# Kernel tuning notes

Measured on AMD Instinct MI355X. Metric: run time of the kernel, lower is better.

The kernel has to match this reference:

```python
import jax, jax.numpy as jnp
import numpy as np

TAU = 1.0
K_TAU = 1.0
MAX_K = 64


def setup_inputs() -> dict:
    key = jax.random.key(0)
    ks = jax.random.split(key, 6)
    B, S, D, H = 8, 4096, 1024, 2048
    token_embeddings = jax.random.normal(ks[0], (B, S, D), dtype=jnp.float32)
    W1 = jax.random.normal(ks[1], (D, H), dtype=jnp.float32) * (1.0 / np.sqrt(D))
    b1 = jnp.zeros((H,), dtype=jnp.float32)
    W2 = jax.random.normal(ks[2], (H, 1), dtype=jnp.float32) * (1.0 / np.sqrt(H))
    b2 = jnp.zeros((1,), dtype=jnp.float32)
    k_logits = jax.random.normal(ks[3], (MAX_K,), dtype=jnp.float32) * 0.02
    return {"token_embeddings": token_embeddings, "W1": W1, "b1": b1,
            "W2": W2, "b2": b2, "k_logits": k_logits}


def _gumbel(rng, shape):
    u = jax.random.uniform(rng, shape, minval=1e-08, maxval=1.0 - 1e-08)
    return -jnp.log(-jnp.log(u))


def reference(token_embeddings, W1, b1, W2, b2, k_logits):
    B, S, D = token_embeddings.shape
    # scorer: Dense -> relu -> Dense(1), squeeze -> [B, S]
    h = jax.nn.relu(jnp.einsum('bsd,dh->bsh', token_embeddings, W1) + b1)
    importance_logits = (jnp.einsum('bsh,ho->bso', h, W2) + b2)[..., 0]

    rng = jax.random.key(42)  # training rng
    rng1, rng2 = jax.random.split(rng)

    # learnable-k selection (training branch)
    k_gumbel = _gumbel(rng1, k_logits.shape)
    k_soft = jax.nn.softmax((k_logits + k_gumbel) / K_TAU)
    expected_k = jnp.sum(k_soft * jnp.arange(1, MAX_K + 1, dtype=k_soft.dtype))
    k_selected = jnp.argmax(k_soft) + 1  # traced int scalar

    # gumbel-softmax hard top-k over tokens
    perturbed = importance_logits + _gumbel(rng2, importance_logits.shape)
    soft_mask = jax.nn.softmax(perturbed / TAU, axis=-1)  # [B, S]
    # rank of each token (0 = smallest); top-k == rank >= S - k
    rank = jnp.argsort(jnp.argsort(soft_mask, axis=-1), axis=-1)
    hard_mask = (rank >= S - k_selected).astype(soft_mask.dtype)
    selection_mask = jax.lax.stop_gradient(hard_mask - soft_mask) + soft_mask

    filtered_embeddings = token_embeddings * selection_mask[..., None]
    return filtered_embeddings, selection_mask, expected_k
```

## Files before the change

kernel.cpp:

```cpp
#include <hip/hip_runtime.h>
#include <stdint.h>

#define B_BATCH 8
#define S_SEQ   4096
#define D_DIM   1024
#define H_DIM   2048
#define M_TOK   (B_BATCH * S_SEQ)
#define MAXK    64
#define NSPLIT  2

typedef unsigned int u32;
typedef unsigned short u16;
typedef unsigned long long u64;
typedef __attribute__((ext_vector_type(8))) short short8;
typedef __attribute__((ext_vector_type(4))) float f32x4;

#define GLOBAL_AS __attribute__((address_space(1)))
#define LDS_AS    __attribute__((address_space(3)))


#define TF_ROUND(x0, x1, r) { x0 += x1; x1 = ((x1 << r) | (x1 >> (32 - r))); x1 ^= x0; }

__device__ __forceinline__ void tf2x32(u32 k0, u32 k1, u32 x0, u32 x1, u32& o0, u32& o1) {
  u32 k2 = k0 ^ k1 ^ 0x1BD11BDAu;
  x0 += k0; x1 += k1;
  TF_ROUND(x0, x1, 13) TF_ROUND(x0, x1, 15) TF_ROUND(x0, x1, 26) TF_ROUND(x0, x1, 6)
  x0 += k1; x1 += k2 + 1u;
  TF_ROUND(x0, x1, 17) TF_ROUND(x0, x1, 29) TF_ROUND(x0, x1, 16) TF_ROUND(x0, x1, 24)
  x0 += k2; x1 += k0 + 2u;
  TF_ROUND(x0, x1, 13) TF_ROUND(x0, x1, 15) TF_ROUND(x0, x1, 26) TF_ROUND(x0, x1, 6)
  x0 += k0; x1 += k1 + 3u;
  TF_ROUND(x0, x1, 17) TF_ROUND(x0, x1, 29) TF_ROUND(x0, x1, 16) TF_ROUND(x0, x1, 24)
  x0 += k1; x1 += k2 + 4u;
  TF_ROUND(x0, x1, 13) TF_ROUND(x0, x1, 15) TF_ROUND(x0, x1, 26) TF_ROUND(x0, x1, 6)
  x0 += k2; x1 += k0 + 5u;
  o0 = x0; o1 = x1;
}

__device__ __forceinline__ void jax_subkeys(u32& r1a, u32& r1b, u32& r2a, u32& r2b) {
  tf2x32(0u, 42u, 0u, 0u, r1a, r1b);
  tf2x32(0u, 42u, 0u, 1u, r2a, r2b);
}

__device__ __forceinline__ u32 jax_bits32(u32 ka, u32 kb, u32 i) {
  u32 o0, o1;
  tf2x32(ka, kb, 0u, i, o0, o1);
  return o0 ^ o1;
}

__device__ __forceinline__ float jax_uniform_from_bits(u32 bits) {
  float f = __uint_as_float((bits >> 9) | 0x3f800000u) - 1.0f;
  float r = f + 1e-8f;
  return fmaxf(1e-8f, r);
}

__device__ __forceinline__ float gumbel_from_bits(u32 bits) {
  float u = jax_uniform_from_bits(bits);
  return -logf(-logf(u));
}

__device__ __forceinline__ u32 ordf(float v) {
  u32 b = __float_as_uint(v);
  return (b & 0x80000000u) ? ~b : (b | 0x80000000u);
}

__device__ __forceinline__ u64 shflx64(u64 v, int m) {
  unsigned lo = (unsigned)v, hi = (unsigned)(v >> 32);
  lo = (unsigned)__shfl_xor((int)lo, m);
  hi = (unsigned)__shfl_xor((int)hi, m);
  return ((u64)hi << 32) | lo;
}


__device__ __forceinline__ u16 f2bf_rn(float x) {
  u32 u = __float_as_uint(x);
  u32 r = u + 0x7fffu + ((u >> 16) & 1u);
  return (u16)(r >> 16);
}

__device__ __forceinline__ void split1(float x, u16& h, u16& lo) {
  h = f2bf_rn(x);
  float hf = __uint_as_float(((u32)h) << 16);
  lo = f2bf_rn(x - hf);
}


__global__ __launch_bounds__(256) void split_a_kernel(const float* __restrict__ x,
                                                      u16* __restrict__ hi,
                                                      u16* __restrict__ lo) {
  const size_t i = ((size_t)blockIdx.x * 256 + threadIdx.x) * 4;
  float4 v = *(const float4*)(x + i);
  u16 h0, h1, h2, h3, l0, l1, l2, l3;
  split1(v.x, h0, l0); split1(v.y, h1, l1); split1(v.z, h2, l2); split1(v.w, h3, l3);
  u64 hv = (u64)h0 | ((u64)h1 << 16) | ((u64)h2 << 32) | ((u64)h3 << 48);
  u64 lv = (u64)l0 | ((u64)l1 << 16) | ((u64)l2 << 32) | ((u64)l3 << 48);
  *(u64*)(hi + i) = hv;
  *(u64*)(lo + i) = lv;
}

__global__ __launch_bounds__(256) void split_w1t_kernel(const float* __restrict__ W1,
                                                        u16* __restrict__ bhi,
                                                        u16* __restrict__ blo) {
  __shared__ float tile[32][33];
  const int tx = threadIdx.x & 31, ty = threadIdx.x >> 5;
  const int n0 = blockIdx.x * 32, k0 = blockIdx.y * 32;
  #pragma unroll
  for (int r = 0; r < 4; ++r)
    tile[ty + r * 8][tx] = W1[(size_t)(k0 + ty + r * 8) * H_DIM + n0 + tx];
  __syncthreads();
  #pragma unroll
  for (int r = 0; r < 4; ++r) {
    const int n = n0 + ty + r * 8, k = k0 + tx;
    u16 h, l;
    split1(tile[tx][ty + r * 8], h, l);
    bhi[(size_t)n * D_DIM + k] = h;
    blo[(size_t)n * D_DIM + k] = l;
  }
}


__device__ __forceinline__ void stage16(const u16* g, u16* l) {
  __builtin_amdgcn_global_load_lds((const GLOBAL_AS u32*)g, (LDS_AS u32*)l, 16, 0, 0);
}

#define WAITV(N) asm volatile("s_waitcnt vmcnt(" #N ")" ::: "memory")
#define FENCE()  asm volatile("" ::: "memory")

__global__ __launch_bounds__(512, 2) void scorer_mfma256(
    const u16* __restrict__ Ahi, const u16* __restrict__ Alo,
    const u16* __restrict__ Bhi, const u16* __restrict__ Blo,
    const float* __restrict__ b1, const float* __restrict__ W2,
    float* __restrict__ pl) {
  extern __shared__ u16 smem[];
  float* red = (float*)(smem + 65536);

  const int tid = threadIdx.x;
  const int w = tid >> 6, l = tid & 63;
  const int wm = w >> 2, wn = w & 3;

  const int b = blockIdx.x;
  const int xcd = b & 7;
  const int nyb = xcd & 1;
  const int m0 = ((b >> 3) * 4 + (xcd >> 1)) * 256;

  const int sig = w * 16 + (l >> 2);
  const int swz = ((l & 3) ^ ((sig >> 1) & 3)) << 3;
  const size_t aoffE = (size_t)(m0 + sig + (sig & 64)) * D_DIM + swz;
  const size_t aoffL = aoffE + (size_t)64 * D_DIM;
  const size_t boff0 = (size_t)(nyb * 1024 + sig) * D_DIM + swz;
  const size_t boff1 = boff0 + (size_t)128 * D_DIM;
  u16* const ldsw = smem + w * 512;

#define ST_AhiE(T) stage16(Ahi + aoffE + (size_t)((((T) & 31) << 5)), ldsw + (((T) & 1) << 15) + 0)
#define ST_AhiL(T) stage16(Ahi + aoffL + (size_t)((((T) & 31) << 5)), ldsw + (((T) & 1) << 15) + 4096)
#define ST_AloE(T) stage16(Alo + aoffE + (size_t)((((T) & 31) << 5)), ldsw + (((T) & 1) << 15) + 8192)
#define ST_AloL(T) stage16(Alo + aoffL + (size_t)((((T) & 31) << 5)), ldsw + (((T) & 1) << 15) + 12288)
#define ST_BhiH0(T) stage16(Bhi + boff0 + ((size_t)((T) >> 5) << 18) + (size_t)((((T) & 31) << 5)), ldsw + (((T) & 1) << 15) + 16384)
#define ST_BhiH1(T) stage16(Bhi + boff1 + ((size_t)((T) >> 5) << 18) + (size_t)((((T) & 31) << 5)), ldsw + (((T) & 1) << 15) + 20480)
#define ST_BloH0(T) stage16(Blo + boff0 + ((size_t)((T) >> 5) << 18) + (size_t)((((T) & 31) << 5)), ldsw + (((T) & 1) << 15) + 24576)
#define ST_BloH1(T) stage16(Blo + boff1 + ((size_t)((T) >> 5) << 18) + (size_t)((((T) & 31) << 5)), ldsw + (((T) & 1) << 15) + 28672)

  int a_off[8], b_off[4];
  #pragma unroll
  for (int mf = 0; mf < 8; ++mf) {
    int slot = wm * 64 + (mf & 3) * 16 + (l & 15);
    a_off[mf] = ((mf >> 2) * 4096) + slot * 32 + (((l >> 4) ^ ((slot >> 1) & 3)) << 3);
  }
  #pragma unroll
  for (int nf = 0; nf < 4; ++nf) {
    int r = wn * 64 + nf * 16 + (l & 15);
    b_off[nf] = r * 32 + (((l >> 4) ^ ((r >> 1) & 3)) << 3);
  }

  f32x4 acc[8][4];
  #pragma unroll
  for (int mf = 0; mf < 8; ++mf)
    #pragma unroll
    for (int nf = 0; nf < 4; ++nf) acc[mf][nf] = (f32x4){0.f, 0.f, 0.f, 0.f};

  const u16* const B0 = smem;
  const u16* const B1 = smem + 32768;
  short8 ah0, ah1, al0, al1, bh[4], bl[4];

#define LDA(BASE, MF) \
  ah0 = *(const short8*)((BASE) + a_off[MF]); \
  ah1 = *(const short8*)((BASE) + a_off[(MF) + 1]); \
  al0 = *(const short8*)((BASE) + 8192 + a_off[MF]); \
  al1 = *(const short8*)((BASE) + 8192 + a_off[(MF) + 1])

#define LDB(BASE) \
  { _Pragma("unroll") \
    for (int nf = 0; nf < 4; ++nf) { \
      bh[nf] = *(const short8*)((BASE) + 16384 + b_off[nf]); \
      bl[nf] = *(const short8*)((BASE) + 24576 + b_off[nf]); \
    } }

#define MMA2(MF) \
  __builtin_amdgcn_s_setprio(1); \
  { _Pragma("unroll") \
    for (int nf = 0; nf < 4; ++nf) { \
      acc[MF][nf] = __builtin_amdgcn_mfma_f32_16x16x32_bf16(ah0, bh[nf], acc[MF][nf], 0, 0, 0); \
      acc[MF][nf] = __builtin_amdgcn_mfma_f32_16x16x32_bf16(ah0, bl[nf], acc[MF][nf], 0, 0, 0); \
      acc[MF][nf] = __builtin_amdgcn_mfma_f32_16x16x32_bf16(al0, bh[nf], acc[MF][nf], 0, 0, 0); \
      acc[(MF) + 1][nf] = __builtin_amdgcn_mfma_f32_16x16x32_bf16(ah1, bh[nf], acc[(MF) + 1][nf], 0, 0, 0); \
      acc[(MF) + 1][nf] = __builtin_amdgcn_mfma_f32_16x16x32_bf16(ah1, bl[nf], acc[(MF) + 1][nf], 0, 0, 0); \
      acc[(MF) + 1][nf] = __builtin_amdgcn_mfma_f32_16x16x32_bf16(al1, bh[nf], acc[(MF) + 1][nf], 0, 0, 0); \
    } } \
  __builtin_amdgcn_s_setprio(0)

  ST_BhiH0(0); ST_BhiH1(0); ST_BloH0(0); ST_BloH1(0);
  ST_AhiE(0);  ST_AloE(0);  ST_AhiL(0);  ST_AloL(0);
  ST_BhiH0(1); ST_BhiH1(1); ST_BloH0(1); ST_BloH1(1);
  ST_AhiE(1);  ST_AloE(1);
  WAITV(8);
  __builtin_amdgcn_s_barrier();
  FENCE();

  for (int it = 0; it < 64; ++it) {
    const bool last = (it == 63);
    const int T1 = 2 * it + 1, T2 = 2 * it + 2, T3 = 2 * it + 3;

    LDB(B0); LDA(B0, 0);
    ST_AhiL(T1); ST_AloL(T1);
    MMA2(0);
    __builtin_amdgcn_s_barrier(); FENCE();
    LDA(B0, 2);
    if (!last) { ST_BhiH0(T2); ST_BhiH1(T2); }
    MMA2(2);
    if (last) { WAITV(8); } else { WAITV(10); }
    __builtin_amdgcn_s_barrier(); FENCE();
    LDA(B0, 4);
    if (!last) { ST_BloH0(T2); ST_BloH1(T2); }
    MMA2(4);
    __builtin_amdgcn_s_barrier(); FENCE();
    LDA(B0, 6);
    if (!last) { ST_AhiE(T2); ST_AloE(T2); }
    MMA2(6);
    if (last) { WAITV(2); } else { WAITV(8); }
    __builtin_amdgcn_s_barrier(); FENCE();
    LDB(B1); LDA(B1, 0);
    if (!last) { ST_AhiL(T2); ST_AloL(T2); }
    MMA2(0);
    __builtin_amdgcn_s_barrier(); FENCE();
    LDA(B1, 2);
    if (!last) { ST_BhiH0(T3); ST_BhiH1(T3); }
    MMA2(2);
    if (last) { WAITV(0); } else { WAITV(10); }
    __builtin_amdgcn_s_barrier(); FENCE();
    LDA(B1, 4);
    if (!last) { ST_BloH0(T3); ST_BloH1(T3); }
    MMA2(4);
    __builtin_amdgcn_s_barrier(); FENCE();
    LDA(B1, 6);
    if (!last) { ST_AhiE(T3); ST_AloE(T3); }
    MMA2(6);

    if ((it & 15) == 15) {
      const int t8 = it >> 4;
      const int nb = nyb * 1024 + t8 * 256 + wn * 64 + (l & 15);
      float b1v[4], w2v[4];
      #pragma unroll
      for (int nf = 0; nf < 4; ++nf) { b1v[nf] = b1[nb + nf * 16]; w2v[nf] = W2[nb + nf * 16]; }
      #pragma unroll
      for (int mf = 0; mf < 8; ++mf)
        #pragma unroll
        for (int r = 0; r < 4; ++r) {
          float p = 0.f;
          #pragma unroll
          for (int nf = 0; nf < 4; ++nf)
            p += fmaxf(acc[mf][nf][r] + b1v[nf], 0.f) * w2v[nf];
          p += __shfl_xor(p, 1); p += __shfl_xor(p, 2);
          p += __shfl_xor(p, 4); p += __shfl_xor(p, 8);
          if ((l & 15) == 0) {
            float* rp = red + ((wm * 128 + mf * 16 + (l >> 4) * 4 + r) << 2) + wn;
            if (t8 == 0) *rp = p; else *rp += p;
          }
        }
      #pragma unroll
      for (int mf = 0; mf < 8; ++mf)
        #pragma unroll
        for (int nf = 0; nf < 4; ++nf) acc[mf][nf] = (f32x4){0.f, 0.f, 0.f, 0.f};
    }

    WAITV(8);
    __builtin_amdgcn_s_barrier(); FENCE();
  }

  __syncthreads();
  if (tid < 256) {
    const float* rp = red + (tid << 2);
    pl[(size_t)nyb * M_TOK + m0 + tid] = rp[0] + rp[1] + rp[2] + rp[3];
  }
}


__global__ __launch_bounds__(256) void scorer_kernel(
    const float* __restrict__ emb, const float* __restrict__ W1,
    const float* __restrict__ b1, const float* __restrict__ W2,
    const float* __restrict__ b2, float* __restrict__ pert) {
  __shared__ float As[16][68];
  __shared__ float Bs[16][132];
  __shared__ float red[64][17];

  const int tid = threadIdx.x;
  const int tx = tid & 15;
  const int ty = tid >> 4;
  const int m0 = blockIdx.x * 64;
  const int at = tid >> 2;
  const int ac = (tid & 3) << 2;
  const int br = tid >> 4;
  const int bc = (tid & 15) << 3;

  float logit[4] = {0.f, 0.f, 0.f, 0.f};

  for (int n0 = 0; n0 < H_DIM; n0 += 128) {
    float acc[4][8];
    #pragma unroll
    for (int i = 0; i < 4; i++)
      #pragma unroll
      for (int j = 0; j < 8; j++) acc[i][j] = 0.f;

    for (int k0 = 0; k0 < D_DIM; k0 += 16) {
      float4 av  = *(const float4*)(emb + (size_t)(m0 + at) * D_DIM + (k0 + ac));
      float4 bv0 = *(const float4*)(W1 + (size_t)(k0 + br) * H_DIM + (n0 + bc));
      float4 bv1 = *(const float4*)(W1 + (size_t)(k0 + br) * H_DIM + (n0 + bc) + 4);
      __syncthreads();
      As[ac + 0][at] = av.x; As[ac + 1][at] = av.y;
      As[ac + 2][at] = av.z; As[ac + 3][at] = av.w;
      *(float4*)&Bs[br][bc]     = bv0;
      *(float4*)&Bs[br][bc + 4] = bv1;
      __syncthreads();
      #pragma unroll
      for (int k = 0; k < 16; k++) {
        float4 a   = *(const float4*)&As[k][ty << 2];
        float4 b0  = *(const float4*)&Bs[k][tx << 3];
        float4 b1v = *(const float4*)&Bs[k][(tx << 3) + 4];
        float aa[4] = {a.x, a.y, a.z, a.w};
        float bb[8] = {b0.x, b0.y, b0.z, b0.w, b1v.x, b1v.y, b1v.z, b1v.w};
        #pragma unroll
        for (int i = 0; i < 4; i++)
          #pragma unroll
          for (int j = 0; j < 8; j++)
            acc[i][j] = fmaf(aa[i], bb[j], acc[i][j]);
      }
    }
    float4 c0 = *(const float4*)(b1 + n0 + (tx << 3));
    float4 c1 = *(const float4*)(b1 + n0 + (tx << 3) + 4);
    float4 w0 = *(const float4*)(W2 + n0 + (tx << 3));
    float4 w1 = *(const float4*)(W2 + n0 + (tx << 3) + 4);
    float cb[8] = {c0.x, c0.y, c0.z, c0.w, c1.x, c1.y, c1.z, c1.w};
    float wb[8] = {w0.x, w0.y, w0.z, w0.w, w1.x, w1.y, w1.z, w1.w};
    #pragma unroll
    for (int i = 0; i < 4; i++)
      #pragma unroll
      for (int j = 0; j < 8; j++) {
        float h = fmaxf(acc[i][j] + cb[j], 0.f);
        logit[i] = fmaf(h, wb[j], logit[i]);
      }
  }

  __syncthreads();
  #pragma unroll
  for (int i = 0; i < 4; i++) red[(ty << 2) + i][tx] = logit[i];
  __syncthreads();

  if (tid < 64) {
    float s = 0.f;
    #pragma unroll
    for (int x = 0; x < 16; x++) s += red[tid][x];
    s += b2[0];
    int t = m0 + tid;
    u32 r1a, r1b, r2a, r2b;
    jax_subkeys(r1a, r1b, r2a, r2b);
    pert[t] = s + gumbel_from_bits(jax_bits32(r2a, r2b, (u32)t));
  }
}


template <bool FROM_PL>
__device__ __forceinline__ void topk_body(const float* kl, const float* pl,
                                          const float* b2, float* mask,
                                          float* expk) {
  const int r = blockIdx.x;
  const int tid = threadIdx.x;
  const int w = tid >> 6, l = tid & 63;
  __shared__ int ksel_sh;
  __shared__ int cnt[2][4];

  u32 r1a, r1b, r2a, r2b;
  jax_subkeys(r1a, r1b, r2a, r2b);

  if (tid < 64) {
    float p = kl[l] + gumbel_from_bits(jax_bits32(r1a, r1b, (u32)l));
    u64 kkey = ((u64)ordf(p) << 32) | (unsigned)(63 - l);
    #pragma unroll
    for (int off = 32; off >= 1; off >>= 1) {
      u64 o = shflx64(kkey, off);
      if (o > kkey) kkey = o;
    }
    if (l == 0) ksel_sh = 64 - (int)(kkey & 0xffffffffu);
    if (r == 0) {
      float m = p;
      #pragma unroll
      for (int off = 32; off >= 1; off >>= 1) m = fmaxf(m, __shfl_xor(m, off));
      float e = expf(p - m);
      float s = e;
      #pragma unroll
      for (int off = 32; off >= 1; off >>= 1) s += __shfl_xor(s, off);
      float v = (e / s) * (float)(l + 1);
      #pragma unroll
      for (int off = 32; off >= 1; off >>= 1) v += __shfl_xor(v, off);
      if (l == 0) expk[0] = v;
    }
  }
  __syncthreads();
  const int k = ksel_sh;
  const float b2v = FROM_PL ? b2[0] : 0.f;

  u64 keys[16];
  #pragma unroll
  for (int j = 0; j < 16; j++) {
    int s = tid + (j << 8);
    int t = (r << 12) + s;
    float v;
    if (FROM_PL) {
      float acc = pl[t];
      #pragma unroll
      for (int q = 1; q < NSPLIT; ++q) acc += pl[(size_t)q * M_TOK + t];
      v = acc + b2v + gumbel_from_bits(jax_bits32(r2a, r2b, (u32)t));
    } else {
      v = mask[t];
    }
    keys[j] = ((u64)ordf(v) << 12) | (unsigned)s;
  }

  u64 lo = 0ull, hi = (1ull << 44) - 1ull;
  int it = 0;
  while (lo < hi) {
    const u64 mid = (lo + hi + 1ull) >> 1;
    int c = 0;
    #pragma unroll
    for (int j = 0; j < 16; j++) c += (keys[j] >= mid) ? 1 : 0;
    #pragma unroll
    for (int off = 32; off >= 1; off >>= 1) c += __shfl_xor(c, off);
    const int buf = it & 1;
    if (l == 0) cnt[buf][w] = c;
    __syncthreads();
    const int tot = cnt[buf][0] + cnt[buf][1] + cnt[buf][2] + cnt[buf][3];
    if (tot >= k) lo = mid; else hi = mid - 1ull;
    ++it;
  }
  const u64 thresh = lo;

  #pragma unroll
  for (int j = 0; j < 16; j++) {
    int s = tid + (j << 8);
    mask[(r << 12) + s] = (keys[j] >= thresh) ? 1.0f : 0.0f;
  }
}

__global__ __launch_bounds__(256) void topk_pl_kernel(const float* __restrict__ kl,
                                                      const float* __restrict__ pl,
                                                      const float* __restrict__ b2,
                                                      float* __restrict__ mask,
                                                      float* __restrict__ expk) {
  topk_body<true>(kl, pl, b2, mask, expk);
}

__global__ __launch_bounds__(256) void topk_kernel(const float* __restrict__ kl,
                                                   float* __restrict__ mask,
                                                   float* __restrict__ expk) {
  topk_body<false>(kl, nullptr, nullptr, mask, expk);
}


__global__ __launch_bounds__(256) void filter_kernel(const float* __restrict__ emb,
                                                     const float* __restrict__ mask,
                                                     float* __restrict__ out) {
  const int t = blockIdx.x;
  const float mk = mask[t];
  const size_t base = (size_t)t * D_DIM + ((size_t)threadIdx.x << 2);
  float4 v = *(const float4*)(emb + base);
  *(float4*)(out + base) = make_float4(v.x * mk, v.y * mk, v.z * mk, v.w * mk);
}


extern "C" void kernel_launch(void* const* d_in, const int* in_sizes, int n_in,
                              void* d_out, int out_size, void* d_ws, size_t ws_size,
                              hipStream_t stream) {
  const float* emb = (const float*)d_in[0];
  const float* W1  = (const float*)d_in[1];
  const float* b1  = (const float*)d_in[2];
  const float* W2  = (const float*)d_in[3];
  const float* b2  = (const float*)d_in[4];
  const float* kl  = (const float*)d_in[5];
  float* out  = (float*)d_out;
  float* mask = out + (size_t)M_TOK * D_DIM;
  float* expk = mask + M_TOK;

  const size_t ws_need = (size_t)H_DIM * D_DIM * 2 * 2 + (size_t)NSPLIT * M_TOK * 4;

  if (ws_size >= ws_need) {
    u16* Ahi = (u16*)d_out;
    u16* Alo = Ahi + (size_t)M_TOK * D_DIM;
    u16* Bhi = (u16*)d_ws;
    u16* Blo = Bhi + (size_t)H_DIM * D_DIM;
    float* pl = (float*)(Blo + (size_t)H_DIM * D_DIM);

    static bool attr_done = false;
    if (!attr_done) {
      hipFuncSetAttribute(reinterpret_cast<const void*>(scorer_mfma256),
                          hipFuncAttributeMaxDynamicSharedMemorySize, 135168);
      attr_done = true;
    }

    split_a_kernel<<<M_TOK * D_DIM / 1024, 256, 0, stream>>>(emb, Ahi, Alo);
    split_w1t_kernel<<<dim3(H_DIM / 32, D_DIM / 32), 256, 0, stream>>>(W1, Bhi, Blo);
    scorer_mfma256<<<256, 512, 135168, stream>>>(Ahi, Alo, Bhi, Blo, b1, W2, pl);
    topk_pl_kernel<<<B_BATCH, 256, 0, stream>>>(kl, pl, b2, mask, expk);
  } else {
    scorer_kernel<<<M_TOK / 64, 256, 0, stream>>>(emb, W1, b1, W2, b2, mask);
    topk_kernel<<<B_BATCH, 256, 0, stream>>>(kl, mask, expk);
  }

  filter_kernel<<<M_TOK, 256, 0, stream>>>(emb, mask, out);
}
```

Baseline: 593.9 us.

## Pre-tile split bf16 operands into LDS-image layout for contiguous staging loads

The split kernels now write the hi/lo bf16 halves of the embeddings and transposed W1 directly in the per-tile, per-wave, swizzled order that the GEMM's LDS buffers use. Each global_load_lds in the scorer then reads a contiguous 8 KB block instead of 16-byte pieces strided by row. The aim is better coalescing and fewer DRAM/L2 transactions in the main GEMM. The cost is more complex index math in the prep kernels, whose reads of A are scattered across rows.

```diff
diff --git a/kernel.cpp b/kernel.cpp
--- a/kernel.cpp
+++ b/kernel.cpp
@@ -85,37 +85,58 @@
 }
 
 
-__global__ __launch_bounds__(256) void split_a_kernel(const float* __restrict__ x,
-                                                      u16* __restrict__ hi,
-                                                      u16* __restrict__ lo) {
-  const size_t i = ((size_t)blockIdx.x * 256 + threadIdx.x) * 4;
-  float4 v = *(const float4*)(x + i);
-  u16 h0, h1, h2, h3, l0, l1, l2, l3;
-  split1(v.x, h0, l0); split1(v.y, h1, l1); split1(v.z, h2, l2); split1(v.w, h3, l3);
-  u64 hv = (u64)h0 | ((u64)h1 << 16) | ((u64)h2 << 32) | ((u64)h3 << 48);
-  u64 lv = (u64)l0 | ((u64)l1 << 16) | ((u64)l2 << 32) | ((u64)l3 << 48);
-  *(u64*)(hi + i) = hv;
-  *(u64*)(lo + i) = lv;
-}
-
-__global__ __launch_bounds__(256) void split_w1t_kernel(const float* __restrict__ W1,
-                                                        u16* __restrict__ bhi,
-                                                        u16* __restrict__ blo) {
-  __shared__ float tile[32][33];
-  const int tx = threadIdx.x & 31, ty = threadIdx.x >> 5;
-  const int n0 = blockIdx.x * 32, k0 = blockIdx.y * 32;
-  #pragma unroll
-  for (int r = 0; r < 4; ++r)
-    tile[ty + r * 8][tx] = W1[(size_t)(k0 + ty + r * 8) * H_DIM + n0 + tx];
+__global__ __launch_bounds__(256) void prep_a_img(const float* __restrict__ x,
+                                                  u16* __restrict__ img) {
+  const u32 t = blockIdx.x * 256 + threadIdx.x;
+  const int idx512 = (int)(t & 511);
+  const int u1 = (int)((t >> 9) & 1);
+  const int kt = (int)((t >> 10) & 31);
+  const int mt = (int)(t >> 15);
+  const int w = idx512 >> 6, l = idx512 & 63;
+  const int sig = w * 16 + (l >> 2);
+  const int r = sig + (sig & 64) + u1 * 64;
+  const int c = (l & 3) ^ ((sig >> 1) & 3);
+  const float* src = x + (size_t)(mt * 256 + r) * D_DIM + kt * 32 + c * 8;
+  float4 v0 = *(const float4*)src;
+  float4 v1 = *(const float4*)(src + 4);
+  union { u16 a[8]; short8 v; } H, L;
+  split1(v0.x, H.a[0], L.a[0]); split1(v0.y, H.a[1], L.a[1]);
+  split1(v0.z, H.a[2], L.a[2]); split1(v0.w, H.a[3], L.a[3]);
+  split1(v1.x, H.a[4], L.a[4]); split1(v1.y, H.a[5], L.a[5]);
+  split1(v1.z, H.a[6], L.a[6]); split1(v1.w, H.a[7], L.a[7]);
+  u16* dhi = img + (size_t)(mt * 32 + kt) * 16384 + u1 * 4096 + idx512 * 8;
+  *(short8*)dhi = H.v;
+  *(short8*)(dhi + 8192) = L.v;
+}
+
+__global__ __launch_bounds__(256) void prep_b_img(const float* __restrict__ W1,
+                                                  u16* __restrict__ img) {
+  __shared__ float tile[64][33];
+  const int tid = threadIdx.x;
+  const int bid = blockIdx.x;
+  const int n0 = (bid & 63) * 32, k0 = (bid >> 6) * 64;
+  const int tx = tid & 31, ty = tid >> 5;
+  #pragma unroll
+  for (int rr = 0; rr < 8; ++rr)
+    tile[ty + rr * 8][tx] = W1[(size_t)(k0 + ty + rr * 8) * H_DIM + n0 + tx];
   __syncthreads();
-  #pragma unroll
-  for (int r = 0; r < 4; ++r) {
-    const int n = n0 + ty + r * 8, k = k0 + tx;
-    u16 h, l;
-    split1(tile[tx][ty + r * 8], h, l);
-    bhi[(size_t)n * D_DIM + k] = h;
-    blo[(size_t)n * D_DIM + k] = l;
-  }
+  const int nc = tid & 31, c8 = tid >> 5;
+  const int ktl = c8 >> 2, cc = c8 & 3;
+  const int n = n0 + nc;
+  const int nyb = n >> 10, t8 = (n >> 8) & 3, rr_ = n & 255;
+  const int hiU = rr_ >> 7;
+  const int sig = rr_ & 127;
+  const int w_ = sig >> 4;
+  const int lpos = (sig & 15) * 4 + (cc ^ ((sig >> 1) & 3));
+  const int kt = (k0 >> 5) + ktl;
+  union { u16 a[8]; short8 v; } H, L;
+  #pragma unroll
+  for (int j = 0; j < 8; ++j)
+    split1(tile[ktl * 32 + cc * 8 + j][nc], H.a[j], L.a[j]);
+  u16* d = img + (size_t)nyb * 2097152 + (size_t)(t8 * 32 + kt) * 16384
+               + hiU * 4096 + w_ * 512 + lpos * 8;
+  *(short8*)d = H.v;
+  *(short8*)(d + 8192) = L.v;
 }
 
 
@@ -127,8 +148,7 @@
 #define FENCE()  asm volatile("" ::: "memory")
 
 __global__ __launch_bounds__(512, 2) void scorer_mfma256(
-    const u16* __restrict__ Ahi, const u16* __restrict__ Alo,
-    const u16* __restrict__ Bhi, const u16* __restrict__ Blo,
+    const u16* __restrict__ Aimg, const u16* __restrict__ Bimg,
     const float* __restrict__ b1, const float* __restrict__ W2,
     float* __restrict__ pl) {
   extern __shared__ u16 smem[];
@@ -141,24 +161,18 @@
   const int b = blockIdx.x;
   const int xcd = b & 7;
   const int nyb = xcd & 1;
-  const int m0 = ((b >> 3) * 4 + (xcd >> 1)) * 256;
-
-  const int sig = w * 16 + (l >> 2);
-  const int swz = ((l & 3) ^ ((sig >> 1) & 3)) << 3;
-  const size_t aoffE = (size_t)(m0 + sig + (sig & 64)) * D_DIM + swz;
-  const size_t aoffL = aoffE + (size_t)64 * D_DIM;
-  const size_t boff0 = (size_t)(nyb * 1024 + sig) * D_DIM + swz;
-  const size_t boff1 = boff0 + (size_t)128 * D_DIM;
+  const int mt = (b >> 3) * 4 + (xcd >> 1);
+  const int m0 = mt * 256;
+
+  const u16* const Amt = Aimg + (size_t)mt * 524288;
+  const u16* const Bny = Bimg + (size_t)nyb * 2097152;
+  const int lane16 = w * 512 + l * 8;
   u16* const ldsw = smem + w * 512;
 
-#define ST_AhiE(T) stage16(Ahi + aoffE + (size_t)((((T) & 31) << 5)), ldsw + (((T) & 1) << 15) + 0)
-#define ST_AhiL(T) stage16(Ahi + aoffL + (size_t)((((T) & 31) << 5)), ldsw + (((T) & 1) << 15) + 4096)
-#define ST_AloE(T) stage16(Alo + aoffE + (size_t)((((T) & 31) << 5)), ldsw + (((T) & 1) << 15) + 8192)
-#define ST_AloL(T) stage16(Alo + aoffL + (size_t)((((T) & 31) << 5)), ldsw + (((T) & 1) << 15) + 12288)
-#define ST_BhiH0(T) stage16(Bhi + boff0 + ((size_t)((T) >> 5) << 18) + (size_t)((((T) & 31) << 5)), ldsw + (((T) & 1) << 15) + 16384)
-#define ST_BhiH1(T) stage16(Bhi + boff1 + ((size_t)((T) >> 5) << 18) + (size_t)((((T) & 31) << 5)), ldsw + (((T) & 1) << 15) + 20480)
-#define ST_BloH0(T) stage16(Blo + boff0 + ((size_t)((T) >> 5) << 18) + (size_t)((((T) & 31) << 5)), ldsw + (((T) & 1) << 15) + 24576)
-#define ST_BloH1(T) stage16(Blo + boff1 + ((size_t)((T) >> 5) << 18) + (size_t)((((T) & 31) << 5)), ldsw + (((T) & 1) << 15) + 28672)
+#define ST_A(T, U) stage16(Amt + (size_t)((((T) & 31) * 16384) + (U) * 4096) + lane16, \
+                           ldsw + (((T) & 1) << 15) + (U) * 4096)
+#define ST_B(T, U) stage16(Bny + (size_t)(((((T) >> 5) * 32 + ((T) & 31)) * 16384) + (U) * 4096) + lane16, \
+                           ldsw + (((T) & 1) << 15) + 16384 + (U) * 4096)
 
   int a_off[8], b_off[4];
   #pragma unroll
@@ -208,10 +222,10 @@
     } } \
   __builtin_amdgcn_s_setprio(0)
 
-  ST_BhiH0(0); ST_BhiH1(0); ST_BloH0(0); ST_BloH1(0);
-  ST_AhiE(0);  ST_AloE(0);  ST_AhiL(0);  ST_AloL(0);
-  ST_BhiH0(1); ST_BhiH1(1); ST_BloH0(1); ST_BloH1(1);
-  ST_AhiE(1);  ST_AloE(1);
+  ST_B(0, 0); ST_B(0, 1); ST_B(0, 2); ST_B(0, 3);
+  ST_A(0, 0); ST_A(0, 2); ST_A(0, 1); ST_A(0, 3);
+  ST_B(1, 0); ST_B(1, 1); ST_B(1, 2); ST_B(1, 3);
+  ST_A(1, 0); ST_A(1, 2);
   WAITV(8);
   __builtin_amdgcn_s_barrier();
   FENCE();
@@ -221,38 +235,38 @@
     const int T1 = 2 * it + 1, T2 = 2 * it + 2, T3 = 2 * it + 3;
 
     LDB(B0); LDA(B0, 0);
-    ST_AhiL(T1); ST_AloL(T1);
+    ST_A(T1, 1); ST_A(T1, 3);
     MMA2(0);
     __builtin_amdgcn_s_barrier(); FENCE();
     LDA(B0, 2);
-    if (!last) { ST_BhiH0(T2); ST_BhiH1(T2); }
+    if (!last) { ST_B(T2, 0); ST_B(T2, 1); }
     MMA2(2);
     if (last) { WAITV(8); } else { WAITV(10); }
     __builtin_amdgcn_s_barrier(); FENCE();
     LDA(B0, 4);
-    if (!last) { ST_BloH0(T2); ST_BloH1(T2); }
+    if (!last) { ST_B(T2, 2); ST_B(T2, 3); }
     MMA2(4);
     __builtin_amdgcn_s_barrier(); FENCE();
     LDA(B0, 6);
-    if (!last) { ST_AhiE(T2); ST_AloE(T2); }
+    if (!last) { ST_A(T2, 0); ST_A(T2, 2); }
     MMA2(6);
     if (last) { WAITV(2); } else { WAITV(8); }
     __builtin_amdgcn_s_barrier(); FENCE();
     LDB(B1); LDA(B1, 0);
-    if (!last) { ST_AhiL(T2); ST_AloL(T2); }
+    if (!last) { ST_A(T2, 1); ST_A(T2, 3); }
     MMA2(0);
     __builtin_amdgcn_s_barrier(); FENCE();
     LDA(B1, 2);
-    if (!last) { ST_BhiH0(T3); ST_BhiH1(T3); }
+    if (!last) { ST_B(T3, 0); ST_B(T3, 1); }
     MMA2(2);
     if (last) { WAITV(0); } else { WAITV(10); }
     __builtin_amdgcn_s_barrier(); FENCE();
     LDA(B1, 4);
-    if (!last) { ST_BloH0(T3); ST_BloH1(T3); }
+    if (!last) { ST_B(T3, 2); ST_B(T3, 3); }
     MMA2(4);
     __builtin_amdgcn_s_barrier(); FENCE();
     LDA(B1, 6);
-    if (!last) { ST_AhiE(T3); ST_AloE(T3); }
+    if (!last) { ST_A(T3, 0); ST_A(T3, 2); }
     MMA2(6);
 
     if ((it & 15) == 15) {
@@ -501,11 +515,9 @@
   const size_t ws_need = (size_t)H_DIM * D_DIM * 2 * 2 + (size_t)NSPLIT * M_TOK * 4;
 
   if (ws_size >= ws_need) {
-    u16* Ahi = (u16*)d_out;
-    u16* Alo = Ahi + (size_t)M_TOK * D_DIM;
-    u16* Bhi = (u16*)d_ws;
-    u16* Blo = Bhi + (size_t)H_DIM * D_DIM;
-    float* pl = (float*)(Blo + (size_t)H_DIM * D_DIM);
+    u16* Aimg = (u16*)d_out;
+    u16* Bimg = (u16*)d_ws;
+    float* pl = (float*)(Bimg + (size_t)2 * H_DIM * D_DIM);
 
     static bool attr_done = false;
     if (!attr_done) {
@@ -514,9 +526,9 @@
       attr_done = true;
     }
 
-    split_a_kernel<<<M_TOK * D_DIM / 1024, 256, 0, stream>>>(emb, Ahi, Alo);
-    split_w1t_kernel<<<dim3(H_DIM / 32, D_DIM / 32), 256, 0, stream>>>(W1, Bhi, Blo);
-    scorer_mfma256<<<256, 512, 135168, stream>>>(Ahi, Alo, Bhi, Blo, b1, W2, pl);
+    prep_a_img<<<16384, 256, 0, stream>>>(emb, Aimg);
+    prep_b_img<<<1024, 256, 0, stream>>>(W1, Bimg);
+    scorer_mfma256<<<256, 512, 135168, stream>>>(Aimg, Bimg, b1, W2, pl);
     topk_pl_kernel<<<B_BATCH, 256, 0, stream>>>(kl, pl, b2, mask, expk);
   } else {
     scorer_kernel<<<M_TOK / 64, 256, 0, stream>>>(emb, W1, b1, W2, b2, mask);
```

Result: no change. 587.5 us (-1.1%).
